# Performance work log

Measured on AMD Instinct MI355X. Metric: run time of the kernel, lower is better.

The kernel has to match this reference:

```python
import jax, jax.numpy as jnp
import numpy as np

N_NODES = 50000
N_EDGES = 1600000
NFEAT, NHID, NCLASS = 512, 256, 40


def _spmm(edge_src, edge_dst, edge_vals, h):
    # out[i] = sum_{e: dst[e]==i} vals[e] * h[src[e]]
    msgs = edge_vals[:, None] * h[edge_src]  # [E, D]
    return jax.ops.segment_sum(msgs, edge_dst, num_segments=h.shape[0])


def _gc(edge_src, edge_dst, edge_vals, x, W, b):
    # GraphConvolution: adj @ (x @ W) + b
    return _spmm(edge_src, edge_dst, edge_vals, x @ W) + b


def setup_inputs() -> dict:
    key = jax.random.key(0)
    ks = jax.random.split(key, 16)
    s = 0.05
    return {
        "x": jax.random.normal(ks[0], (N_NODES, NFEAT), jnp.float32),
        "edge_src": jax.random.randint(ks[1], (N_EDGES,), 0, N_NODES, jnp.int32),
        "edge_dst": jax.random.randint(ks[2], (N_EDGES,), 0, N_NODES, jnp.int32),
        "edge_vals": jax.random.uniform(ks[3], (N_EDGES,), jnp.float32),
        "W0": jax.random.normal(ks[4], (NFEAT, NHID), jnp.float32) * s,
        "b0": jax.random.normal(ks[5], (NHID,), jnp.float32) * s,
        "W1": jax.random.normal(ks[6], (NFEAT, NHID), jnp.float32) * s,
        "b1": jax.random.normal(ks[7], (NHID,), jnp.float32) * s,
        "W2": jax.random.normal(ks[8], (NHID, NHID), jnp.float32) * s,
        "b2": jax.random.normal(ks[9], (NHID,), jnp.float32) * s,
        "W3": jax.random.normal(ks[10], (NHID, NHID), jnp.float32) * s,
        "b3": jax.random.normal(ks[11], (NHID,), jnp.float32) * s,
        "W5": jax.random.normal(ks[12], (4 * NHID, NCLASS), jnp.float32) * s,
        "b5": jax.random.normal(ks[13], (NCLASS,), jnp.float32) * s,
    }


def reference(x, edge_src, edge_dst, edge_vals, W0, b0, W1, b1, W2, b2, W3, b3, W5, b5):
    z = x @ W0 + b0
    x1 = jax.nn.relu(_gc(edge_src, edge_dst, edge_vals, x, W1, b1)) + z
    # NOTE: the original module applies gc2 (same weights) twice; gc4 is unused.
    x2 = jax.nn.relu(_gc(edge_src, edge_dst, edge_vals, x1, W2, b2)) + x1
    x3 = jax.nn.relu(_gc(edge_src, edge_dst, edge_vals, x2, W2, b2)) + x2
    x4 = jax.nn.relu(_gc(edge_src, edge_dst, edge_vals, x3, W3, b3)) + x3
    xc = jnp.concatenate((x4, x3, x2, x1), axis=1)  # [N, 4*nhid]
    # dropout is identity in eval mode
    x5 = _gc(edge_src, edge_dst, edge_vals, xc, W5, b5)
    return jax.nn.log_softmax(x5, axis=1)
```

## Files before the change

### kernel.cpp

```cpp
#include <hip/hip_runtime.h>
#include <hip/hip_fp16.h>
#include <math.h>
#include <stdint.h>

#define N_NODES 50000
#define N_EDGES 1600000
#define NFEAT 512
#define NHID 256
#define NCLASS 40
#define MPAD 50048
#define NPART 8
#define ROWS_PER_PART 6250
#define PCAP 212992
#define EPB 4096
#define BPP 128
#define NBLK 196
#define SLICE_STRIDE ((size_t)MPAD * 32)
#define CEV_CAP 6144

typedef _Float16 half8 __attribute__((ext_vector_type(8)));
typedef float floatx4 __attribute__((ext_vector_type(4)));

__device__ __forceinline__ void gload_lds16(const void* g, void* l) {
    __builtin_amdgcn_global_load_lds((const __attribute__((address_space(1))) void*)g,
                                     (__attribute__((address_space(3))) void*)l, 16, 0, 0);
}

__device__ __forceinline__ float cev_val(unsigned ev) {
    return (float)__builtin_bit_cast(_Float16, (unsigned short)(ev >> 16));
}


__global__ void zero_i32(int* __restrict__ p, int n) {
    int i = blockIdx.x * blockDim.x + threadIdx.x;
    if (i < n) p[i] = 0;
}

__global__ __launch_bounds__(256) void bin_kernel(const int* __restrict__ esrc,
                                                  const int* __restrict__ edst,
                                                  const float* __restrict__ evals,
                                                  int* __restrict__ cnt,
                                                  int* __restrict__ pcount,
                                                  uint2* __restrict__ plist) {
    __shared__ int lcnt[NPART], lbase[NPART], lcur[NPART];
    int base = blockIdx.x * EPB;
    int n = min(EPB, N_EDGES - base);
    if (threadIdx.x < NPART) lcnt[threadIdx.x] = 0;
    __syncthreads();
    for (int i = threadIdx.x; i < n; i += 256) {
        int d = edst[base + i];
        atomicAdd(&lcnt[d / ROWS_PER_PART], 1);
        atomicAdd(&cnt[d], 1);
    }
    __syncthreads();
    if (threadIdx.x < NPART) {
        lbase[threadIdx.x] = atomicAdd(&pcount[threadIdx.x], lcnt[threadIdx.x]);
        lcur[threadIdx.x] = 0;
    }
    __syncthreads();
    for (int i = threadIdx.x; i < n; i += 256) {
        int d = edst[base + i];
        int p = d / ROWS_PER_PART;
        int o = atomicAdd(&lcur[p], 1);
        int s = esrc[base + i];
        plist[(size_t)p * PCAP + lbase[p] + o] =
            make_uint2((unsigned)((d << 16) | s), __float_as_uint(evals[base + i]));
    }
}

__global__ __launch_bounds__(1024) void exscan4_kernel(const int* __restrict__ cnt,
                                                       int* __restrict__ rowptr,
                                                       int* __restrict__ cursor, int n) {
    __shared__ int wsum[16];
    __shared__ int carry_s;
    const int tid = threadIdx.x;
    const int lane = tid & 63;
    const int wid = tid >> 6;
    if (tid == 0) carry_s = 0;
    __syncthreads();
    for (int base = 0; base < n; base += 4096) {
        int i0 = base + tid * 4;
        int4 v = make_int4(0, 0, 0, 0);
        if (i0 + 3 < n) {
            v = *(const int4*)(cnt + i0);
        } else {
            if (i0 + 0 < n) v.x = cnt[i0 + 0];
            if (i0 + 1 < n) v.y = cnt[i0 + 1];
            if (i0 + 2 < n) v.z = cnt[i0 + 2];
        }
        int s = v.x + v.y + v.z + v.w;
        int sc = s;
        #pragma unroll
        for (int off = 1; off < 64; off <<= 1) {
            int t = __shfl_up(sc, off);
            if (lane >= off) sc += t;
        }
        if (lane == 63) wsum[wid] = sc;
        __syncthreads();
        if (wid == 0) {
            int ws = (lane < 16) ? wsum[lane] : 0;
            #pragma unroll
            for (int off = 1; off < 16; off <<= 1) {
                int t = __shfl_up(ws, off);
                if (lane >= off) ws += t;
            }
            if (lane < 16) wsum[lane] = ws;
        }
        __syncthreads();
        int ex = carry_s + (wid ? wsum[wid - 1] : 0) + sc - s;
        int p0 = ex, p1 = ex + v.x, p2 = p1 + v.y, p3 = p2 + v.z;
        if (i0 + 0 < n) { rowptr[i0 + 0] = p0; if (cursor) cursor[i0 + 0] = p0; }
        if (i0 + 1 < n) { rowptr[i0 + 1] = p1; if (cursor) cursor[i0 + 1] = p1; }
        if (i0 + 2 < n) { rowptr[i0 + 2] = p2; if (cursor) cursor[i0 + 2] = p2; }
        if (i0 + 3 < n) { rowptr[i0 + 3] = p3; if (cursor) cursor[i0 + 3] = p3; }
        __syncthreads();
        if (tid == 0) carry_s += wsum[15];
        __syncthreads();
    }
    if (tid == 0) rowptr[n] = carry_s;
}

__global__ __launch_bounds__(1024) void exscan4g_kernel(const int* __restrict__ cnt,
                                                        const int* __restrict__ order,
                                                        int* __restrict__ rowptr,
                                                        int* __restrict__ cursor, int n) {
    __shared__ int wsum[16];
    __shared__ int carry_s;
    const int tid = threadIdx.x;
    const int lane = tid & 63;
    const int wid = tid >> 6;
    if (tid == 0) carry_s = 0;
    __syncthreads();
    for (int base = 0; base < n; base += 4096) {
        int i0 = base + tid * 4;
        int4 v = make_int4(0, 0, 0, 0);
        if (i0 + 0 < n) v.x = cnt[order[i0 + 0]];
        if (i0 + 1 < n) v.y = cnt[order[i0 + 1]];
        if (i0 + 2 < n) v.z = cnt[order[i0 + 2]];
        if (i0 + 3 < n) v.w = cnt[order[i0 + 3]];
        int s = v.x + v.y + v.z + v.w;
        int sc = s;
        #pragma unroll
        for (int off = 1; off < 64; off <<= 1) {
            int t = __shfl_up(sc, off);
            if (lane >= off) sc += t;
        }
        if (lane == 63) wsum[wid] = sc;
        __syncthreads();
        if (wid == 0) {
            int ws = (lane < 16) ? wsum[lane] : 0;
            #pragma unroll
            for (int off = 1; off < 16; off <<= 1) {
                int t = __shfl_up(ws, off);
                if (lane >= off) ws += t;
            }
            if (lane < 16) wsum[lane] = ws;
        }
        __syncthreads();
        int ex = carry_s + (wid ? wsum[wid - 1] : 0) + sc - s;
        int p0 = ex, p1 = ex + v.x, p2 = p1 + v.y, p3 = p2 + v.z;
        if (i0 + 0 < n) { rowptr[i0 + 0] = p0; cursor[i0 + 0] = p0; }
        if (i0 + 1 < n) { rowptr[i0 + 1] = p1; cursor[i0 + 1] = p1; }
        if (i0 + 2 < n) { rowptr[i0 + 2] = p2; cursor[i0 + 2] = p2; }
        if (i0 + 3 < n) { rowptr[i0 + 3] = p3; cursor[i0 + 3] = p3; }
        __syncthreads();
        if (tid == 0) carry_s += wsum[15];
        __syncthreads();
    }
    if (tid == 0) rowptr[n] = carry_s;
}


__global__ __launch_bounds__(256) void sort_hist_kernel(const int* __restrict__ cnt,
                                                        int* __restrict__ gh) {
    __shared__ int lbin[256];
    int t = threadIdx.x;
    lbin[t] = 0;
    __syncthreads();
    int i = blockIdx.x * 256 + t;
    if (i < N_NODES) atomicAdd(&lbin[255 - min(cnt[i], 255)], 1);
    __syncthreads();
    gh[t * NBLK + blockIdx.x] = lbin[t];
}

__global__ __launch_bounds__(256) void sort_scatter_kernel(const int* __restrict__ cnt,
                                                           const int* __restrict__ ghx,
                                                           int* __restrict__ order,
                                                           int* __restrict__ rank) {
    __shared__ int lbase[256], lcnt2[256];
    int t = threadIdx.x;
    lbase[t] = ghx[t * NBLK + blockIdx.x];
    lcnt2[t] = 0;
    __syncthreads();
    int i = blockIdx.x * 256 + t;
    if (i < N_NODES) {
        int bin = 255 - min(cnt[i], 255);
        int my = atomicAdd(&lcnt2[bin], 1);
        int pos = lbase[bin] + my;
        order[pos] = i;
        rank[i] = pos;
    }
}

__global__ __launch_bounds__(256) void pscatter_kernel(const int* __restrict__ pcount,
                                                       const uint2* __restrict__ plist,
                                                       const int* __restrict__ rank,
                                                       int* __restrict__ cursor,
                                                       unsigned* __restrict__ cev) {
    int part = blockIdx.x & (NPART - 1);
    int bip = blockIdx.x >> 3;
    int n = pcount[part];
    const uint2* lp = plist + (size_t)part * PCAP;
    for (int i = bip * 256 + threadIdx.x; i < n; i += BPP * 256) {
        uint2 r = lp[i];
        int d = r.x >> 16;
        int s = r.x & 0xFFFF;
        int pos = atomicAdd(&cursor[rank[d]], 1);
        unsigned short hb = __builtin_bit_cast(unsigned short, (_Float16)__uint_as_float(r.y));
        cev[pos] = ((unsigned)hb << 16) | (unsigned)rank[s];
    }
}


__global__ void conv_w_kernel(const float* __restrict__ W, _Float16* __restrict__ BT,
                              int K, int N, int Npad) {
    int id = blockIdx.x * blockDim.x + threadIdx.x;
    if (id >= Npad * K) return;
    int n = id / K;
    int k = id - n * K;
    BT[id] = (n < N) ? (_Float16)W[(size_t)k * N + n] : (_Float16)0.f;
}

__global__ __launch_bounds__(256) void conv_xs(const float* __restrict__ x,
                                               const int* __restrict__ rank,
                                               _Float16* __restrict__ xh) {
    int id = blockIdx.x * 256 + threadIdx.x;
    int node = id >> 6;
    int kc = (id & 63) * 8;
    if (node >= MPAD) return;
    half8 h;
    if (node < N_NODES) {
        const float4* p = (const float4*)(x + (size_t)node * NFEAT + kc);
        float4 a = p[0], b = p[1];
        h[0] = (_Float16)a.x; h[1] = (_Float16)a.y; h[2] = (_Float16)a.z; h[3] = (_Float16)a.w;
        h[4] = (_Float16)b.x; h[5] = (_Float16)b.y; h[6] = (_Float16)b.z; h[7] = (_Float16)b.w;
        int pos = rank[node];
        __builtin_nontemporal_store(h, (half8*)(xh + (size_t)pos * NFEAT + kc));
    } else {
        #pragma unroll
        for (int j = 0; j < 8; ++j) h[j] = (_Float16)0.f;
        *(half8*)(xh + (size_t)node * NFEAT + kc) = h;
    }
}


__global__ __launch_bounds__(256, 2)
void gemm_x16(const _Float16* __restrict__ A, const _Float16* __restrict__ BT,
              const float* __restrict__ bias1,
              _Float16* __restrict__ out1, _Float16* __restrict__ out2) {
    __shared__ _Float16 As[128 * 64];
    __shared__ _Float16 Bs[128 * 64];

    const int tid = threadIdx.x;
    const int w = tid >> 6;
    const int lane = tid & 63;
    const int row0 = blockIdx.y * 128;
    const int col0 = blockIdx.x * 128;

    const int wr = w >> 1;
    const int wc = w & 1;
    const int mi = lane & 15;
    const int ksel = lane >> 4;

    const int srow = lane >> 3;
    const int scol = ((lane & 7) ^ srow) << 3;

    floatx4 acc[4][4];
    #pragma unroll
    for (int i = 0; i < 4; ++i)
        #pragma unroll
        for (int j = 0; j < 4; ++j)
            acc[i][j] = (floatx4)0.f;

    for (int k0 = 0; k0 < NFEAT; k0 += 64) {
        #pragma unroll
        for (int j = 0; j < 4; ++j) {
            int rowblk = (j * 4 + w) * 8;
            const _Float16* src = A + (size_t)(row0 + rowblk + srow) * NFEAT + k0 + scol;
            gload_lds16(src, (char*)As + rowblk * 128);
        }
        #pragma unroll
        for (int j = 0; j < 4; ++j) {
            int nblk = (j * 4 + w) * 8;
            const _Float16* src = BT + (size_t)(col0 + nblk + srow) * NFEAT + k0 + scol;
            gload_lds16(src, (char*)Bs + nblk * 128);
        }
        asm volatile("s_waitcnt vmcnt(0)" ::: "memory");
        __syncthreads();

        half8 a[2][4];
        half8 b[2][4];
        #pragma unroll
        for (int kk = 0; kk < 2; ++kk) {
            int kb = kk * 64 + (ksel << 4);
            #pragma unroll
            for (int fm = 0; fm < 4; ++fm) {
                int r = wr * 64 + fm * 16 + mi;
                int byte = kb ^ ((r & 7) << 4);
                a[kk][fm] = *(const half8*)((const char*)As + r * 128 + byte);
            }
            #pragma unroll
            for (int fn = 0; fn < 4; ++fn) {
                int n = wc * 64 + fn * 16 + mi;
                int byte = kb ^ ((n & 7) << 4);
                b[kk][fn] = *(const half8*)((const char*)Bs + n * 128 + byte);
            }
        }
        #pragma unroll
        for (int kk = 0; kk < 2; ++kk)
            #pragma unroll
            for (int fm = 0; fm < 4; ++fm)
                #pragma unroll
                for (int fn = 0; fn < 4; ++fn)
                    acc[fm][fn] = __builtin_amdgcn_mfma_f32_16x16x32_f16(
                        a[kk][fm], b[kk][fn], acc[fm][fn], 0, 0, 0);
        __syncthreads();
    }

    #pragma unroll
    for (int fm = 0; fm < 4; ++fm) {
        #pragma unroll
        for (int fn = 0; fn < 4; ++fn) {
            #pragma unroll
            for (int r = 0; r < 4; ++r) {
                int gr = row0 + wr * 64 + fm * 16 + (lane >> 4) * 4 + r;
                int gc = col0 + wc * 64 + fn * 16 + (lane & 15);
                if (gr < N_NODES) {
                    float v = acc[fm][fn][r];
                    if (gc < 256) {
                        out1[(size_t)(gc >> 5) * SLICE_STRIDE + (size_t)gr * 32 + (gc & 31)] =
                            (_Float16)(v + bias1[gc]);
                    } else {
                        int gc2 = gc - 256;
                        out2[(size_t)(gc2 >> 5) * SLICE_STRIDE + (size_t)gr * 32 + (gc2 & 31)] =
                            (_Float16)v;
                    }
                }
            }
        }
    }
}


template<int BN, bool OUTS>
__global__ __launch_bounds__(256, 2)
void gemm_f16(const _Float16* __restrict__ A0, const _Float16* __restrict__ A1,
              const _Float16* __restrict__ A2, const _Float16* __restrict__ A3,
              int kPerPart, int K,
              const _Float16* __restrict__ BT,
              _Float16* __restrict__ out1, int M, int N) {
    constexpr int WN = BN / 2;
    constexpr int FN = WN / 16;
    __shared__ _Float16 As[128 * 64];
    __shared__ _Float16 Bs[BN * 64];

    const int tid = threadIdx.x;
    const int w = tid >> 6;
    const int lane = tid & 63;
    const int row0 = blockIdx.y * 128;
    const int col0 = blockIdx.x * BN;

    const int wr = w >> 1;
    const int wc = w & 1;
    const int mi = lane & 15;
    const int ksel = lane >> 4;

    const int srow = lane >> 3;
    const int gsw = (lane & 7) ^ srow;

    floatx4 acc[4][FN];
    #pragma unroll
    for (int i = 0; i < 4; ++i)
        #pragma unroll
        for (int j = 0; j < FN; ++j)
            acc[i][j] = (floatx4)0.f;

    for (int k0 = 0; k0 < K; k0 += 64) {
        int part = k0 / kPerPart;
        int kloc = k0 - part * kPerPart;
        const _Float16* Ap = (part == 0) ? A0 : (part == 1) ? A1 : (part == 2) ? A2 : A3;
        int sA0 = kloc >> 5;

        #pragma unroll
        for (int j = 0; j < 4; ++j) {
            int chunk = j * 4 + w;
            int r = chunk * 8 + srow;
            const _Float16* src = Ap + (size_t)(sA0 + (gsw >> 2)) * SLICE_STRIDE
                                + (size_t)(row0 + r) * 32 + (gsw & 3) * 8;
            gload_lds16(src, (char*)As + chunk * 1024);
        }
        #pragma unroll
        for (int j = 0; j < BN / 32; ++j) {
            int nblk = (j * 4 + w) * 8;
            const _Float16* src = BT + (size_t)(col0 + nblk + srow) * K + k0 + ((lane & 7) ^ srow) * 8;
            gload_lds16(src, (char*)Bs + nblk * 128);
        }
        asm volatile("s_waitcnt vmcnt(0)" ::: "memory");
        __syncthreads();

        half8 a[2][4];
        half8 b[2][FN];
        #pragma unroll
        for (int kk = 0; kk < 2; ++kk) {
            int kb = kk * 64 + (ksel << 4);
            #pragma unroll
            for (int fm = 0; fm < 4; ++fm) {
                int r = wr * 64 + fm * 16 + mi;
                int byte = kb ^ ((r & 7) << 4);
                a[kk][fm] = *(const half8*)((const char*)As + r * 128 + byte);
            }
            #pragma unroll
            for (int fn = 0; fn < FN; ++fn) {
                int n = wc * WN + fn * 16 + mi;
                int byte = kb ^ ((n & 7) << 4);
                b[kk][fn] = *(const half8*)((const char*)Bs + n * 128 + byte);
            }
        }
        #pragma unroll
        for (int kk = 0; kk < 2; ++kk)
            #pragma unroll
            for (int fm = 0; fm < 4; ++fm)
                #pragma unroll
                for (int fn = 0; fn < FN; ++fn)
                    acc[fm][fn] = __builtin_amdgcn_mfma_f32_16x16x32_f16(
                        a[kk][fm], b[kk][fn], acc[fm][fn], 0, 0, 0);
        __syncthreads();
    }

    #pragma unroll
    for (int fm = 0; fm < 4; ++fm) {
        #pragma unroll
        for (int fn = 0; fn < FN; ++fn) {
            #pragma unroll
            for (int r = 0; r < 4; ++r) {
                int gr = row0 + wr * 64 + fm * 16 + (lane >> 4) * 4 + r;
                int gc = col0 + wc * WN + fn * 16 + (lane & 15);
                if (gr < M && gc < N) {
                    float v = acc[fm][fn][r];
                    if (OUTS) {
                        out1[(size_t)(gc >> 5) * SLICE_STRIDE + (size_t)gr * 32 + (gc & 31)] =
                            (_Float16)v;
                    } else {
                        out1[(size_t)gr * N + gc] = (_Float16)v;
                    }
                }
            }
        }
    }
}


#define SPMM_EDGE_LOOP(EVSRC)                                                     \
    for (int e = 0; __any(e < deg); e += 8) {                                     \
        unsigned ev[8];                                                           \
        _Pragma("unroll")                                                         \
        for (int u = 0; u < 8; ++u) {                                             \
            int ee = e + u;                                                       \
            ev[u] = EVSRC(begs + (ee < deg ? ee : 0));                            \
        }                                                                         \
        uint4 hw[8];                                                              \
        _Pragma("unroll")                                                         \
        for (int u = 0; u < 8; ++u)                                               \
            hw[u] = *(const uint4*)(Y + (size_t)(ev[u] & 0xFFFF) * 32);           \
        _Pragma("unroll")                                                         \
        for (int u = 0; u < 8; ++u) {                                             \
            unsigned short vb = (e + u < deg) ? (unsigned short)(ev[u] >> 16)     \
                                              : (unsigned short)0;                \
            __half vh = __builtin_bit_cast(__half, vb);                           \
            __half2 vv = __half2half2(vh);                                        \
            ac0 = __hfma2(vv, __builtin_bit_cast(__half2, hw[u].x), ac0);         \
            ac1 = __hfma2(vv, __builtin_bit_cast(__half2, hw[u].y), ac1);         \
            ac2 = __hfma2(vv, __builtin_bit_cast(__half2, hw[u].z), ac2);         \
            ac3 = __hfma2(vv, __builtin_bit_cast(__half2, hw[u].w), ac3);         \
        }                                                                         \
    }

__global__ __launch_bounds__(256) void spmm_epi_sl(const int* __restrict__ rowptr,
                                                   const unsigned* __restrict__ cev,
                                                   const _Float16* __restrict__ Ysl,
                                                   const float* __restrict__ bias,
                                                   const _Float16* __restrict__ ressl,
                                                   _Float16* __restrict__ outsl) {
    __shared__ unsigned sev[CEV_CAP];
    __shared__ int srp[65];
    const int tid = threadIdx.x;
    const int w = tid >> 6;
    const int lane = tid & 63;
    const int slice = blockIdx.x & 7;
    const int rb = (blockIdx.x >> 3) * 64;

    if (tid < 65) srp[tid] = rowptr[min(rb + tid, N_NODES)];
    __syncthreads();
    const int ebase = srp[0];
    const int ecnt = srp[64] - ebase;
    const int nstage = min(ecnt, CEV_CAP);
    for (int i = tid; i < nstage; i += 256) sev[i] = cev[ebase + i];
    __syncthreads();

    const int lrow = w * 16 + (lane >> 2);
    const int rowIdx = rb + lrow;
    const int fl = (lane & 3) * 8;
    const _Float16* Y = Ysl + (size_t)slice * SLICE_STRIDE + fl;

    bool active = rowIdx < N_NODES;
    int deg = srp[lrow + 1] - srp[lrow];
    int begs = (deg > 0) ? (srp[lrow] - ebase) : 0;

    __half2 ac0 = __float2half2_rn(0.f), ac1 = ac0, ac2 = ac0, ac3 = ac0;
    if (ecnt <= CEV_CAP) {
        #define EV_LDS(i) sev[(i)]
        SPMM_EDGE_LOOP(EV_LDS)
        #undef EV_LDS
    } else {
        #define EV_GLB(i) cev[ebase + (i)]
        SPMM_EDGE_LOOP(EV_GLB)
        #undef EV_GLB
    }
    if (active) {
        int col = slice * 32 + fl;
        float4 bb0 = *(const float4*)(bias + col);
        float4 bb1 = *(const float4*)(bias + col + 4);
        size_t ro = (size_t)slice * SLICE_STRIDE + (size_t)rowIdx * 32 + fl;
        half8 rr = __builtin_nontemporal_load((const half8*)(ressl + ro));
        float2 f0 = __half22float2(ac0), f1 = __half22float2(ac1);
        float2 f2 = __half22float2(ac2), f3 = __half22float2(ac3);
        half8 o;
        o[0] = (_Float16)(fmaxf(f0.x + bb0.x, 0.f) + (float)rr[0]);
        o[1] = (_Float16)(fmaxf(f0.y + bb0.y, 0.f) + (float)rr[1]);
        o[2] = (_Float16)(fmaxf(f1.x + bb0.z, 0.f) + (float)rr[2]);
        o[3] = (_Float16)(fmaxf(f1.y + bb0.w, 0.f) + (float)rr[3]);
        o[4] = (_Float16)(fmaxf(f2.x + bb1.x, 0.f) + (float)rr[4]);
        o[5] = (_Float16)(fmaxf(f2.y + bb1.y, 0.f) + (float)rr[5]);
        o[6] = (_Float16)(fmaxf(f3.x + bb1.z, 0.f) + (float)rr[6]);
        o[7] = (_Float16)(fmaxf(f3.y + bb1.w, 0.f) + (float)rr[7]);
        __builtin_nontemporal_store(o, (half8*)(outsl + ro));
    }
}


__global__ __launch_bounds__(256) void spmm40_lsm(const int* __restrict__ rowptr,
                                                  const int* __restrict__ order,
                                                  const unsigned* __restrict__ cev,
                                                  const _Float16* __restrict__ Y5,
                                                  const float* __restrict__ bias,
                                                  float* __restrict__ out) {
    int rowIdx = (blockIdx.x * blockDim.x + threadIdx.x) >> 6;
    if (rowIdx >= N_NODES) return;
    int lane = threadIdx.x & 63;
    bool act = lane < NCLASS;
    const _Float16* Yl = Y5 + lane;
    int row = order[rowIdx];
    int beg = rowptr[rowIdx];
    int end = rowptr[rowIdx + 1];
    float acc = 0.f;
    int e = beg;
    for (; e + 8 <= end; e += 8) {
        unsigned ev[8];
        #pragma unroll
        for (int j = 0; j < 8; ++j) ev[j] = cev[e + j];
        float h[8];
        #pragma unroll
        for (int j = 0; j < 8; ++j)
            h[j] = act ? (float)Yl[(size_t)(ev[j] & 0xFFFF) * NCLASS] : 0.f;
        #pragma unroll
        for (int j = 0; j < 8; ++j) acc = fmaf(cev_val(ev[j]), h[j], acc);
    }
    for (; e < end; ++e) {
        unsigned ev = cev[e];
        float h = act ? (float)Yl[(size_t)(ev & 0xFFFF) * NCLASS] : 0.f;
        acc = fmaf(cev_val(ev), h, acc);
    }
    float x = act ? (acc + bias[lane]) : -INFINITY;
    float m = x;
    #pragma unroll
    for (int off = 32; off > 0; off >>= 1) m = fmaxf(m, __shfl_xor(m, off));
    float ex = act ? __expf(x - m) : 0.f;
    float ssum = ex;
    #pragma unroll
    for (int off = 32; off > 0; off >>= 1) ssum += __shfl_xor(ssum, off);
    float ls = logf(ssum);
    if (act) out[(size_t)row * NCLASS + lane] = x - m - ls;
}


extern "C" void kernel_launch(void* const* d_in, const int* in_sizes, int n_in,
                              void* d_out, int out_size, void* d_ws, size_t ws_size,
                              hipStream_t stream) {
    const float* x     = (const float*)d_in[0];
    const int*   esrc  = (const int*)d_in[1];
    const int*   edst  = (const int*)d_in[2];
    const float* evals = (const float*)d_in[3];
    const float* W0 = (const float*)d_in[4];
    const float* b0 = (const float*)d_in[5];
    const float* W1 = (const float*)d_in[6];
    const float* b1 = (const float*)d_in[7];
    const float* W2 = (const float*)d_in[8];
    const float* b2 = (const float*)d_in[9];
    const float* W3 = (const float*)d_in[10];
    const float* b3 = (const float*)d_in[11];
    const float* W5 = (const float*)d_in[12];
    const float* b5 = (const float*)d_in[13];
    float* out = (float*)d_out;

    char* ws = (char*)d_ws;
    size_t off = 0;
    auto alloc = [&](size_t bytes) {
        char* p = ws + off;
        off = (off + bytes + 255) & ~(size_t)255;
        return p;
    };
    const size_t SLB = 2ull * 8 * SLICE_STRIDE;
    _Float16* xh   = (_Float16*)alloc(2ull * MPAD * NFEAT);
    _Float16* zh   = (_Float16*)alloc(SLB);
    _Float16* Yh   = (_Float16*)alloc(SLB);
    _Float16* x1h  = (_Float16*)alloc(SLB);
    _Float16* x2h  = (_Float16*)alloc(SLB);
    _Float16* x3h  = (_Float16*)alloc(SLB);
    _Float16* x4h  = (_Float16*)alloc(SLB);
    _Float16* Y5h  = (_Float16*)alloc(2ull * N_NODES * NCLASS);
    _Float16* BT01 = (_Float16*)alloc(2ull * 512 * NFEAT);
    _Float16* BT2  = (_Float16*)alloc(2ull * NHID * NHID);
    _Float16* BT3  = (_Float16*)alloc(2ull * NHID * NHID);
    _Float16* BT5  = (_Float16*)alloc(2ull * 64 * 1024);
    int* cnt    = (int*)alloc(sizeof(int) * (N_NODES + NPART));
    int* pcount = cnt + N_NODES;
    int* gh     = (int*)alloc(sizeof(int) * (NBLK * 256));
    int* ghx    = (int*)alloc(sizeof(int) * (NBLK * 256 + 1));
    int* order  = (int*)alloc(sizeof(int) * N_NODES);
    int* rank   = (int*)alloc(sizeof(int) * N_NODES);
    int* rowptr = (int*)alloc(sizeof(int) * (N_NODES + 1));
    int* cursor = (int*)alloc(sizeof(int) * N_NODES);
    uint2* plist = (uint2*)alloc(8ull * NPART * PCAP);
    unsigned* cev = (unsigned*)alloc(4ull * N_EDGES + 256);
    (void)ws_size;

    zero_i32<<<(N_NODES + NPART + 255) / 256, 256, 0, stream>>>(cnt, N_NODES + NPART);
    bin_kernel<<<(N_EDGES + EPB - 1) / EPB, 256, 0, stream>>>(esrc, edst, evals, cnt, pcount, plist);
    sort_hist_kernel<<<NBLK, 256, 0, stream>>>(cnt, gh);
    exscan4_kernel<<<1, 1024, 0, stream>>>(gh, ghx, nullptr, NBLK * 256);
    sort_scatter_kernel<<<NBLK, 256, 0, stream>>>(cnt, ghx, order, rank);
    exscan4g_kernel<<<1, 1024, 0, stream>>>(cnt, order, rowptr, cursor, N_NODES);
    pscatter_kernel<<<NPART * BPP, 256, 0, stream>>>(pcount, plist, rank, cursor, cev);

    conv_xs<<<MPAD / 4, 256, 0, stream>>>(x, rank, xh);
    conv_w_kernel<<<(256 * NFEAT + 255) / 256, 256, 0, stream>>>(W0, BT01, NFEAT, NHID, NHID);
    conv_w_kernel<<<(256 * NFEAT + 255) / 256, 256, 0, stream>>>(W1, BT01 + 256 * NFEAT, NFEAT, NHID, NHID);
    conv_w_kernel<<<(NHID * NHID + 255) / 256, 256, 0, stream>>>(W2, BT2, NHID, NHID, NHID);
    conv_w_kernel<<<(NHID * NHID + 255) / 256, 256, 0, stream>>>(W3, BT3, NHID, NHID, NHID);
    conv_w_kernel<<<(64 * 1024 + 255) / 256, 256, 0, stream>>>(W5, BT5, 1024, NCLASS, 64);

    const int mtiles = MPAD / 128;
    const int spmmGrid = ((N_NODES + 63) / 64) * 8;
    dim3 blk(256);

    gemm_x16<<<dim3(4, mtiles), blk, 0, stream>>>(xh, BT01, b0, zh, Yh);
    spmm_epi_sl<<<spmmGrid, blk, 0, stream>>>(rowptr, cev, Yh, b1, zh, x1h);

    gemm_f16<128, true><<<dim3(2, mtiles), blk, 0, stream>>>(x1h, x1h, x1h, x1h, NHID, NHID, BT2, Yh, N_NODES, NHID);
    spmm_epi_sl<<<spmmGrid, blk, 0, stream>>>(rowptr, cev, Yh, b2, x1h, x2h);

    gemm_f16<128, true><<<dim3(2, mtiles), blk, 0, stream>>>(x2h, x2h, x2h, x2h, NHID, NHID, BT2, Yh, N_NODES, NHID);
    spmm_epi_sl<<<spmmGrid, blk, 0, stream>>>(rowptr, cev, Yh, b2, x2h, x3h);

    gemm_f16<128, true><<<dim3(2, mtiles), blk, 0, stream>>>(x3h, x3h, x3h, x3h, NHID, NHID, BT3, Yh, N_NODES, NHID);
    spmm_epi_sl<<<spmmGrid, blk, 0, stream>>>(rowptr, cev, Yh, b3, x3h, x4h);

    gemm_f16<64, false><<<dim3(1, mtiles), blk, 0, stream>>>(x4h, x3h, x2h, x1h, NHID, 4 * NHID, BT5, Y5h, N_NODES, NCLASS);

    spmm40_lsm<<<(N_NODES * 64 + 255) / 256, blk, 0, stream>>>(rowptr, order, cev, Y5h, b5, out);
}
```

Baseline: 769.2 us.

## Bin edges by sorted-row edge offset after ranking, with wave-aggregated LDS atomics

Edge preprocessing is reordered. A plain histogram kernel now computes degrees first. After the degree sort and scan, a new binning pass partitions edges by the CSR edge offset of their ranked destination (rowptr/PEDGE), so each of the 8 partitions holds a balanced contiguous range of the output. Inside that pass, per-partition offsets come from ballot/popcount aggregation, which replaces one LDS atomic per edge, and the src/dst ranks are stored already applied, so the scatter pass no longer does rank lookups. The cost is reading the edge arrays once more and a separate launch for the histogram.

```diff
diff --git a/kernel.cpp b/kernel.cpp
--- a/kernel.cpp
+++ b/kernel.cpp
@@ -10,9 +10,9 @@
 #define NCLASS 40
 #define MPAD 50048
 #define NPART 8
-#define ROWS_PER_PART 6250
+#define PEDGE 200000
 #define PCAP 212992
-#define EPB 4096
+#define EPB2 1024
 #define BPP 128
 #define NBLK 196
 #define SLICE_STRIDE ((size_t)MPAD * 32)
@@ -36,36 +36,10 @@
     if (i < n) p[i] = 0;
 }
 
-__global__ __launch_bounds__(256) void bin_kernel(const int* __restrict__ esrc,
-                                                  const int* __restrict__ edst,
-                                                  const float* __restrict__ evals,
-                                                  int* __restrict__ cnt,
-                                                  int* __restrict__ pcount,
-                                                  uint2* __restrict__ plist) {
-    __shared__ int lcnt[NPART], lbase[NPART], lcur[NPART];
-    int base = blockIdx.x * EPB;
-    int n = min(EPB, N_EDGES - base);
-    if (threadIdx.x < NPART) lcnt[threadIdx.x] = 0;
-    __syncthreads();
-    for (int i = threadIdx.x; i < n; i += 256) {
-        int d = edst[base + i];
-        atomicAdd(&lcnt[d / ROWS_PER_PART], 1);
-        atomicAdd(&cnt[d], 1);
-    }
-    __syncthreads();
-    if (threadIdx.x < NPART) {
-        lbase[threadIdx.x] = atomicAdd(&pcount[threadIdx.x], lcnt[threadIdx.x]);
-        lcur[threadIdx.x] = 0;
-    }
-    __syncthreads();
-    for (int i = threadIdx.x; i < n; i += 256) {
-        int d = edst[base + i];
-        int p = d / ROWS_PER_PART;
-        int o = atomicAdd(&lcur[p], 1);
-        int s = esrc[base + i];
-        plist[(size_t)p * PCAP + lbase[p] + o] =
-            make_uint2((unsigned)((d << 16) | s), __float_as_uint(evals[base + i]));
-    }
+__global__ void hist_kernel(const int* __restrict__ dst, int* __restrict__ cnt) {
+    int i = blockIdx.x * blockDim.x + threadIdx.x;
+    int stride = gridDim.x * blockDim.x;
+    for (; i < N_EDGES; i += stride) atomicAdd(&cnt[dst[i]], 1);
 }
 
 __global__ __launch_bounds__(1024) void exscan4_kernel(const int* __restrict__ cnt,
@@ -202,22 +176,72 @@
     }
 }
 
-__global__ __launch_bounds__(256) void pscatter_kernel(const int* __restrict__ pcount,
-                                                       const uint2* __restrict__ plist,
-                                                       const int* __restrict__ rank,
-                                                       int* __restrict__ cursor,
-                                                       unsigned* __restrict__ cev) {
+
+__global__ __launch_bounds__(256) void bin2_kernel(const int* __restrict__ esrc,
+                                                   const int* __restrict__ edst,
+                                                   const float* __restrict__ evals,
+                                                   const int* __restrict__ rank,
+                                                   const int* __restrict__ rowptr,
+                                                   int* __restrict__ pcount,
+                                                   uint2* __restrict__ plist) {
+    __shared__ int lcnt[NPART], lbase[NPART], lcur[NPART];
+    const int base = blockIdx.x * EPB2;
+    const int n = min(EPB2, N_EDGES - base);
+    const int tid = threadIdx.x;
+    const int lane = tid & 63;
+    if (tid < NPART) { lcnt[tid] = 0; lcur[tid] = 0; }
+    __syncthreads();
+    for (int i = tid; i < n; i += 256) {
+        int rd = rank[edst[base + i]];
+        int p = rowptr[rd] / PEDGE;
+        atomicAdd(&lcnt[p], 1);
+    }
+    __syncthreads();
+    if (tid < NPART) lbase[tid] = atomicAdd(&pcount[tid], lcnt[tid]);
+    __syncthreads();
+    const int nceil = (n + 255) & ~255;
+    for (int i = tid; i < nceil; i += 256) {
+        bool on = i < n;
+        int d = 0, s = 0; float v = 0.f;
+        if (on) { d = edst[base + i]; s = esrc[base + i]; v = evals[base + i]; }
+        int rd = on ? rank[d] : 0;
+        int rs = on ? rank[s] : 0;
+        int p = on ? (rowptr[rd] / PEDGE) : NPART;
+        int mybase = 0, myoff = 0;
+        #pragma unroll
+        for (int q = 0; q < NPART; ++q) {
+            unsigned long long mq = __ballot(p == q);
+            int cq = __popcll(mq);
+            int wbq = 0;
+            if (lane == q && cq > 0) wbq = atomicAdd(&lcur[q], cq);
+            wbq = __shfl(wbq, q);
+            if (p == q) {
+                mybase = wbq;
+                myoff = __popcll(mq & ((1ull << lane) - 1ull));
+            }
+        }
+        if (on) {
+            plist[(size_t)p * PCAP + lbase[p] + mybase + myoff] =
+                make_uint2(((unsigned)rd << 16) | (unsigned)rs, __float_as_uint(v));
+        }
+    }
+}
+
+__global__ __launch_bounds__(256) void pscatter2_kernel(const int* __restrict__ pcount,
+                                                        const uint2* __restrict__ plist,
+                                                        int* __restrict__ cursor,
+                                                        unsigned* __restrict__ cev) {
     int part = blockIdx.x & (NPART - 1);
     int bip = blockIdx.x >> 3;
     int n = pcount[part];
     const uint2* lp = plist + (size_t)part * PCAP;
     for (int i = bip * 256 + threadIdx.x; i < n; i += BPP * 256) {
         uint2 r = lp[i];
-        int d = r.x >> 16;
-        int s = r.x & 0xFFFF;
-        int pos = atomicAdd(&cursor[rank[d]], 1);
+        int rd = r.x >> 16;
+        int rs = r.x & 0xFFFF;
+        int pos = atomicAdd(&cursor[rd], 1);
         unsigned short hb = __builtin_bit_cast(unsigned short, (_Float16)__uint_as_float(r.y));
-        cev[pos] = ((unsigned)hb << 16) | (unsigned)rank[s];
+        cev[pos] = ((unsigned)hb << 16) | (unsigned)rs;
     }
 }
 
@@ -645,12 +669,13 @@
     (void)ws_size;
 
     zero_i32<<<(N_NODES + NPART + 255) / 256, 256, 0, stream>>>(cnt, N_NODES + NPART);
-    bin_kernel<<<(N_EDGES + EPB - 1) / EPB, 256, 0, stream>>>(esrc, edst, evals, cnt, pcount, plist);
+    hist_kernel<<<2048, 256, 0, stream>>>(edst, cnt);
     sort_hist_kernel<<<NBLK, 256, 0, stream>>>(cnt, gh);
     exscan4_kernel<<<1, 1024, 0, stream>>>(gh, ghx, nullptr, NBLK * 256);
     sort_scatter_kernel<<<NBLK, 256, 0, stream>>>(cnt, ghx, order, rank);
     exscan4g_kernel<<<1, 1024, 0, stream>>>(cnt, order, rowptr, cursor, N_NODES);
-    pscatter_kernel<<<NPART * BPP, 256, 0, stream>>>(pcount, plist, rank, cursor, cev);
+    bin2_kernel<<<(N_EDGES + EPB2 - 1) / EPB2, 256, 0, stream>>>(esrc, edst, evals, rank, rowptr, pcount, plist);
+    pscatter2_kernel<<<NPART * BPP, 256, 0, stream>>>(pcount, plist, cursor, cev);
 
     conv_xs<<<MPAD / 4, 256, 0, stream>>>(x, rank, xh);
     conv_w_kernel<<<(256 * NFEAT + 255) / 256, 256, 0, stream>>>(W0, BT01, NFEAT, NHID, NHID);
```

Result: slower. 816.1 us (+6.1%).
